# Optimization experiments

Hardware: AMD Instinct MI355X
Metric: run time of the kernel (lower is better)

Reference implementation:

```python
import jax, jax.numpy as jnp
import numpy as np
from functools import partial

NUM_PARTS = 6      # k clusters (PCB-style parts)
N_ITERS = 25       # fixed Lloyd iteration count (original uses tol=1e-4; fixed iters for jit/diff)


def _kmeans_single(points, k, n_iters):
    """Lloyd's k-means on points [N, D]; returns centers [k, D].
    Deterministic init: first k points (stand-in for the original's random init)."""
    centers0 = points[:k]  # [k, D]
    pt_sq = jnp.sum(points * points, axis=-1, keepdims=True)  # [N, 1]

    def step(centers, _):
        # squared euclidean distances [N, k] via GEMM
        c_sq = jnp.sum(centers * centers, axis=-1)            # [k]
        d = pt_sq - 2.0 * (points @ centers.T) + c_sq[None, :]
        assign = jnp.argmin(d, axis=-1)                       # [N]
        onehot = jax.nn.one_hot(assign, k, dtype=points.dtype)  # [N, k]
        counts = jnp.sum(onehot, axis=0)                      # [k]
        sums = onehot.T @ points                              # [k, D]
        new_centers = sums / jnp.maximum(counts, 1.0)[:, None]
        # keep old center for empty clusters
        new_centers = jnp.where(counts[:, None] > 0, new_centers, centers)
        return new_centers, None

    centers, _ = jax.lax.scan(step, centers0, None, length=n_iters)
    return centers  # [k, D]


def setup_inputs() -> dict:
    key = jax.random.key(0)
    x = jax.random.normal(key, (64, 2048, 24, 12), dtype=jnp.float32)
    return {"x": x}


def reference(x):
    B, C = x.shape[0], x.shape[1]
    pts = x.reshape(B, C, -1).transpose(0, 2, 1)              # [B, N=H*W, C]
    centers = jax.vmap(partial(_kmeans_single, k=NUM_PARTS, n_iters=N_ITERS))(pts)  # [B, k, C]
    clus = centers.transpose(0, 2, 1)[:, :, :, None]          # [B, C, k, 1]
    return clus
```

## Files before the change

### kernel.cpp

```cpp
#include <hip/hip_runtime.h>

#define NPTS 288
#define DIMS 2048
#define KC   6
#define N_IT 25

#define GT   96
#define KB   32
#define KSPL 2
#define KPS  (DIMS / KSPL)
#define NCH  (KPS / KB)
#define NTP  6

#define GLD16(gp, lp) __builtin_amdgcn_global_load_lds(                      \
    (const __attribute__((address_space(1))) void*)(gp),                     \
    (__attribute__((address_space(3))) void*)(lp), 16, 0, 0)

__global__ __launch_bounds__(256, 2) void k_gram(const float* __restrict__ x,
                                                 float* __restrict__ Gp, int nb) {
  const int bid = blockIdx.x;
  const int b  = bid / (NTP * KSPL);
  const int r0 = bid - b * (NTP * KSPL);
  const int ks = r0 / NTP, pr = r0 - ks * NTP;
  const int ti = (pr < 3) ? 0 : ((pr < 5) ? 1 : 2);
  const int tj = (pr < 3) ? pr : ((pr < 5) ? (pr - 2) : 2);
  const int t = threadIdx.x;
  const int tr = t >> 4, tc = t & 15;
  const int w = t >> 6, l = t & 63;
  const float* __restrict__ xb = x + (size_t)b * (DIMS * NPTS);
  float* __restrict__ Gb = Gp + ((size_t)ks * nb + b) * (NPTS * NPTS);

  __shared__ __attribute__((aligned(16))) float bufA[2][KB][GT];
  __shared__ __attribute__((aligned(16))) float bufB[2][KB][GT];

  int off[3];
#pragma unroll
  for (int iq = 0; iq < 3; ++iq) {
    const int e = (w * 3 + iq) * 256 + 4 * l;
    off[iq] = (e / GT) * NPTS + (e - (e / GT) * GT);
  }
  const float* __restrict__ baseA = xb + (size_t)(ks * KPS) * NPTS + ti * GT;
  const float* __restrict__ baseB = xb + (size_t)(ks * KPS) * NPTS + tj * GT;

  float acc[6][6];
#pragma unroll
  for (int ii = 0; ii < 6; ++ii)
#pragma unroll
    for (int jj = 0; jj < 6; ++jj) acc[ii][jj] = 0.f;

  auto stage = [&](int n, int c) {
#pragma unroll
    for (int iq = 0; iq < 3; ++iq) {
      const int o   = off[iq] + c * (KB * NPTS);
      const int lw  = (w * 3 + iq) * 256;
      GLD16(baseA + o, &bufA[n][0][0] + lw);
      GLD16(baseB + o, &bufB[n][0][0] + lw);
    }
  };

  stage(0, 0);
  __syncthreads();
  int n = 0;
  for (int c = 0; c < NCH; ++c) {
    if (c + 1 < NCH) stage(n ^ 1, c + 1);
#pragma unroll
    for (int kk = 0; kk < KB; ++kk) {
      float af[6], bf[6];
      const float2 a01 = *(const float2*)&bufA[n][kk][6 * tr];
      const float2 a23 = *(const float2*)&bufA[n][kk][6 * tr + 2];
      const float2 a45 = *(const float2*)&bufA[n][kk][6 * tr + 4];
      const float2 b01 = *(const float2*)&bufB[n][kk][6 * tc];
      const float2 b23 = *(const float2*)&bufB[n][kk][6 * tc + 2];
      const float2 b45 = *(const float2*)&bufB[n][kk][6 * tc + 4];
      af[0] = a01.x; af[1] = a01.y; af[2] = a23.x; af[3] = a23.y; af[4] = a45.x; af[5] = a45.y;
      bf[0] = b01.x; bf[1] = b01.y; bf[2] = b23.x; bf[3] = b23.y; bf[4] = b45.x; bf[5] = b45.y;
#pragma unroll
      for (int ii = 0; ii < 6; ++ii)
#pragma unroll
        for (int jj = 0; jj < 6; ++jj) acc[ii][jj] += af[ii] * bf[jj];
    }
    __syncthreads();
    n ^= 1;
  }

#pragma unroll
  for (int ii = 0; ii < 6; ++ii) {
    const int ri = ti * GT + 6 * tr + ii;
#pragma unroll
    for (int jj = 0; jj < 6; ++jj)
      Gb[(size_t)ri * NPTS + tj * GT + 6 * tc + jj] = acc[ii][jj];
  }
}

__global__ __launch_bounds__(256) void k_gsum(const float* __restrict__ Gp,
                                              float* __restrict__ G, int nb) {
  const size_t N2  = (size_t)NPTS * NPTS;
  const size_t tot = (size_t)nb * N2;
  const size_t p1  = (size_t)nb * N2;
  for (size_t e = (size_t)blockIdx.x * 256 + threadIdx.x; e < tot;
       e += (size_t)gridDim.x * 256) {
    const size_t b = e / N2;
    const int rc = (int)(e - b * N2);
    const int r = rc / NPTS, c = rc - r * NPTS;
    const int src_rc = ((r / GT) <= (c / GT)) ? rc : (c * NPTS + r);
    const size_t src = b * N2 + (size_t)src_rc;
    G[e] = Gp[src] + Gp[p1 + src];
  }
}

__global__ __launch_bounds__(1024) void k_lloyd(const float* __restrict__ G,
                                                float* __restrict__ wg, int nb) {
  const int b = blockIdx.x;
  const int t = threadIdx.x, wv = t >> 6, lane = t & 63;
  const float* __restrict__ Gb = G + (size_t)b * (NPTS * NPTS);

  __shared__ float w2[NPTS][8];
  __shared__ float pool[KC][NPTS][5];
  __shared__ float u[KC][NPTS];
  __shared__ int assign_s[NPTS];
  __shared__ float csq[KC];
  __shared__ int cnt_i[KC];

  for (int e = t; e < NPTS * 8; e += 1024) {
    const int i = e >> 3, k = e & 7;
    w2[i][k] = (k < KC && i == k) ? 1.f : 0.f;
  }
  __syncthreads();

  for (int it = 0; it < N_IT; ++it) {
    {
      const int jg = t / 320;
      const int i  = t - jg * 320;
      if (t < 960 && i < NPTS) {
        float a0 = 0, a1 = 0, a2 = 0, a3 = 0, a4 = 0, a5 = 0;
        const float* __restrict__ gp = Gb + (size_t)(jg * 96) * NPTS + i;
        for (int jj = 0; jj < 96; ++jj) {
          const float g = gp[(size_t)jj * NPTS];
          const int j = jg * 96 + jj;
          const float4 wA = *(const float4*)&w2[j][0];
          const float2 wB = *(const float2*)&w2[j][4];
          a0 += wA.x * g; a1 += wA.y * g; a2 += wA.z * g;
          a3 += wA.w * g; a4 += wB.x * g; a5 += wB.y * g;
        }
        pool[0][i][jg] = a0; pool[1][i][jg] = a1; pool[2][i][jg] = a2;
        pool[3][i][jg] = a3; pool[4][i][jg] = a4; pool[5][i][jg] = a5;
      }
    }
    __syncthreads();
    for (int e = t; e < KC * NPTS; e += 1024) {
      const int k = e / NPTS, i = e - k * NPTS;
      u[k][i] = pool[k][i][0] + pool[k][i][1] + pool[k][i][2];
    }
    if (t >= 960 && t < 960 + KC) cnt_i[t - 960] = 0;
    __syncthreads();
    if (wv < KC) {
      float s = 0.f;
      for (int i = lane; i < NPTS; i += 64) s += w2[i][wv] * u[wv][i];
#pragma unroll
      for (int off = 32; off; off >>= 1) s += __shfl_xor(s, off, 64);
      if (lane == 0) csq[wv] = s;
    }
    __syncthreads();
    int myA = -1;
    if (t < NPTS) {
      float best = 0.f;
      int bi = 0;
#pragma unroll
      for (int k = 0; k < KC; ++k) {
        const float sc = 0.5f * csq[k] - u[k][t];
        if (k == 0 || sc < best) { best = sc; bi = k; }
      }
      assign_s[t] = bi;
      myA = bi;
    }
    if (t < 320) {
#pragma unroll
      for (int k = 0; k < KC; ++k) {
        unsigned long long m = __ballot(myA == k);
        if (lane == 0) atomicAdd(&cnt_i[k], (int)__popcll(m));
      }
    }
    __syncthreads();
    if (t < NPTS) {
      const int a = assign_s[t];
#pragma unroll
      for (int k = 0; k < KC; ++k) {
        const int cn = cnt_i[k];
        if (cn > 0) w2[t][k] = (a == k) ? (1.0f / (float)cn) : 0.f;
      }
    }
    __syncthreads();
  }

  for (int e = t; e < NPTS * 8; e += 1024)
    wg[(size_t)b * (NPTS * 8) + e] = w2[e >> 3][e & 7];
}

__global__ __launch_bounds__(1024) void k_cent(const float* __restrict__ x,
                                               const float* __restrict__ wg,
                                               float* __restrict__ out, int nb) {
  const int b = blockIdx.x >> 3, s = blockIdx.x & 7;
  const int t = threadIdx.x, wv = t >> 6, lane = t & 63;
  const float* __restrict__ Mb = x + (size_t)b * (DIMS * NPTS);

  __shared__ float tile[64 * 145];
  __shared__ float pool[KC][64][17];
  __shared__ float w2[NPTS][8];

  for (int e = t; e < NPTS * 8; e += 1024)
    w2[e >> 3][e & 7] = wg[(size_t)b * (NPTS * 8) + e];

  for (int dt = 0; dt < 4; ++dt) {
    float a0 = 0, a1 = 0, a2 = 0, a3 = 0, a4 = 0, a5 = 0;
#pragma unroll
    for (int h = 0; h < 2; ++h) {
      __syncthreads();
#pragma unroll
      for (int i = 0; i < 9; ++i) {
        const int e = t + 1024 * i;
        const int d = e / 144, j = e - d * 144;
        tile[d * 145 + j] = Mb[(size_t)(s * 256 + dt * 64 + d) * NPTS + h * 144 + j];
      }
      __syncthreads();
      const int base = lane * 145 + wv * 9;
#pragma unroll
      for (int r = 0; r < 9; ++r) {
        const float p = tile[base + r];
        const int j = h * 144 + wv * 9 + r;
        const float4 wA = *(const float4*)&w2[j][0];
        const float2 wB = *(const float2*)&w2[j][4];
        a0 += wA.x * p; a1 += wA.y * p; a2 += wA.z * p;
        a3 += wA.w * p; a4 += wB.x * p; a5 += wB.y * p;
      }
    }
    pool[0][lane][wv] = a0; pool[1][lane][wv] = a1; pool[2][lane][wv] = a2;
    pool[3][lane][wv] = a3; pool[4][lane][wv] = a4; pool[5][lane][wv] = a5;
    __syncthreads();
    if (t < KC * 64) {
      const int d = t / KC, k = t - d * KC;
      float sum = 0.f;
#pragma unroll
      for (int w = 0; w < 16; ++w) sum += pool[k][d][w];
      out[((size_t)b * DIMS + s * 256 + dt * 64 + d) * KC + k] = sum;
    }
    __syncthreads();
  }
}

extern "C" void kernel_launch(void* const* d_in, const int* in_sizes, int n_in,
                              void* d_out, int out_size, void* d_ws, size_t ws_size,
                              hipStream_t stream) {
  const float* x = (const float*)d_in[0];
  float* out     = (float*)d_out;
  const int nb   = in_sizes[0] / (DIMS * NPTS);
  const size_t N2 = (size_t)NPTS * NPTS;

  float* Gp = (float*)d_ws;
  float* G  = Gp + (size_t)KSPL * nb * N2;
  float* wg = G + (size_t)nb * N2;

  hipLaunchKernelGGL(k_gram,  dim3(nb * NTP * KSPL), dim3(256),  0, stream, x, Gp, nb);
  hipLaunchKernelGGL(k_gsum,  dim3(4096),            dim3(256),  0, stream, Gp, G, nb);
  hipLaunchKernelGGL(k_lloyd, dim3(nb),              dim3(1024), 0, stream, G, wg, nb);
  hipLaunchKernelGGL(k_cent,  dim3(nb * 8),          dim3(1024), 0, stream, x, wg, out, nb);
}
```

Baseline: 475.8 us.

## Tile-based Gram symmetrization and assignment-indexed accumulation in Lloyd loop

k_gsum now works per 96x96 upper tile: it sums the split-K partials, writes the tile and writes its transpose through an LDS buffer, in place of a grid-stride loop with divides. The Lloyd matvec replaces the weight-matrix multiply with per-cluster accumulation keyed on a wave-uniform assignment (readfirstlane), and normalizes by precomputed reciprocal counts. The first iteration reads Gram columns directly. This relies on the assignment loaded being uniform across the wave, and on the hidden code staying consistent with the new count and normalization handling.

```diff
diff --git a/kernel.cpp b/kernel.cpp
--- a/kernel.cpp
+++ b/kernel.cpp
@@ -94,17 +94,35 @@
 
 __global__ __launch_bounds__(256) void k_gsum(const float* __restrict__ Gp,
                                               float* __restrict__ G, int nb) {
-  const size_t N2  = (size_t)NPTS * NPTS;
-  const size_t tot = (size_t)nb * N2;
-  const size_t p1  = (size_t)nb * N2;
-  for (size_t e = (size_t)blockIdx.x * 256 + threadIdx.x; e < tot;
-       e += (size_t)gridDim.x * 256) {
-    const size_t b = e / N2;
-    const int rc = (int)(e - b * N2);
-    const int r = rc / NPTS, c = rc - r * NPTS;
-    const int src_rc = ((r / GT) <= (c / GT)) ? rc : (c * NPTS + r);
-    const size_t src = b * N2 + (size_t)src_rc;
-    G[e] = Gp[src] + Gp[p1 + src];
+  const int bid = blockIdx.x;
+  const int b = bid / NTP, pr = bid - b * NTP;
+  const int ti = (pr < 3) ? 0 : ((pr < 5) ? 1 : 2);
+  const int tj = (pr < 3) ? pr : ((pr < 5) ? (pr - 2) : 2);
+  const int t = threadIdx.x;
+  const size_t N2 = (size_t)NPTS * NPTS;
+  const size_t p1 = (size_t)nb * N2;
+  const float* __restrict__ s0 = Gp + (size_t)b * N2;
+  const float* __restrict__ s1 = Gp + p1 + (size_t)b * N2;
+  float* __restrict__ Gb = G + (size_t)b * N2;
+
+  __shared__ float tl[GT * 97];
+
+#pragma unroll
+  for (int q = 0; q < 36; ++q) {
+    const int e = q * 256 + t;
+    const int lr = e / GT, lc = e - lr * GT;
+    const size_t idx = (size_t)(ti * GT + lr) * NPTS + tj * GT + lc;
+    const float v = s0[idx] + s1[idx];
+    Gb[idx] = v;
+    tl[lr * 97 + lc] = v;
+  }
+  if (ti == tj) return;
+  __syncthreads();
+#pragma unroll
+  for (int q = 0; q < 36; ++q) {
+    const int e = q * 256 + t;
+    const int lr = e / GT, lc = e - lr * GT;
+    Gb[(size_t)(tj * GT + lr) * NPTS + ti * GT + lc] = tl[lc * 97 + lr];
   }
 }
 
@@ -116,10 +134,12 @@
 
   __shared__ float w2[NPTS][8];
   __shared__ float pool[KC][NPTS][5];
-  __shared__ float u[KC][NPTS];
+  __shared__ float u[NPTS * KC > 0 ? KC : KC][NPTS];
   __shared__ int assign_s[NPTS];
   __shared__ float csq[KC];
   __shared__ int cnt_i[KC];
+  __shared__ float rn_s[KC];
+  __shared__ int live_s[KC];
 
   for (int e = t; e < NPTS * 8; e += 1024) {
     const int i = e >> 3, k = e & 7;
@@ -128,31 +148,50 @@
   __syncthreads();
 
   for (int it = 0; it < N_IT; ++it) {
-    {
+    if (t < KC) {
+      const int cn = cnt_i[t];
+      live_s[t] = (cn > 0) ? 1 : 0;
+      rn_s[t]   = (cn > 0) ? (1.0f / (float)cn) : 0.f;
+      cnt_i[t] = 0;
+    }
+    __syncthreads();
+
+    if (it == 0) {
+      if (t < NPTS) {
+#pragma unroll
+        for (int k = 0; k < KC; ++k) u[k][t] = Gb[(size_t)t * NPTS + k];
+      }
+    } else {
       const int jg = t / 320;
       const int i  = t - jg * 320;
       if (t < 960 && i < NPTS) {
-        float a0 = 0, a1 = 0, a2 = 0, a3 = 0, a4 = 0, a5 = 0;
+        float s0 = 0, s1 = 0, s2 = 0, s3 = 0, s4 = 0, s5 = 0;
         const float* __restrict__ gp = Gb + (size_t)(jg * 96) * NPTS + i;
+        const int jb = jg * 96;
         for (int jj = 0; jj < 96; ++jj) {
           const float g = gp[(size_t)jj * NPTS];
-          const int j = jg * 96 + jj;
-          const float4 wA = *(const float4*)&w2[j][0];
-          const float2 wB = *(const float2*)&w2[j][4];
-          a0 += wA.x * g; a1 += wA.y * g; a2 += wA.z * g;
-          a3 += wA.w * g; a4 += wB.x * g; a5 += wB.y * g;
+          const int a = __builtin_amdgcn_readfirstlane(assign_s[jb + jj]);
+          if      (a == 0) s0 += g;
+          else if (a == 1) s1 += g;
+          else if (a == 2) s2 += g;
+          else if (a == 3) s3 += g;
+          else if (a == 4) s4 += g;
+          else             s5 += g;
         }
-        pool[0][i][jg] = a0; pool[1][i][jg] = a1; pool[2][i][jg] = a2;
-        pool[3][i][jg] = a3; pool[4][i][jg] = a4; pool[5][i][jg] = a5;
-      }
-    }
-    __syncthreads();
-    for (int e = t; e < KC * NPTS; e += 1024) {
-      const int k = e / NPTS, i = e - k * NPTS;
-      u[k][i] = pool[k][i][0] + pool[k][i][1] + pool[k][i][2];
-    }
-    if (t >= 960 && t < 960 + KC) cnt_i[t - 960] = 0;
-    __syncthreads();
+        pool[0][i][jg] = s0; pool[1][i][jg] = s1; pool[2][i][jg] = s2;
+        pool[3][i][jg] = s3; pool[4][i][jg] = s4; pool[5][i][jg] = s5;
+      }
+    }
+    __syncthreads();
+    if (it > 0) {
+      for (int e = t; e < KC * NPTS; e += 1024) {
+        const int k = e / NPTS, i = e - k * NPTS;
+        if (live_s[k])
+          u[k][i] = (pool[k][i][0] + pool[k][i][1] + pool[k][i][2]) * rn_s[k];
+      }
+      __syncthreads();
+    }
+
     if (wv < KC) {
       float s = 0.f;
       for (int i = lane; i < NPTS; i += 64) s += w2[i][wv] * u[wv][i];
@@ -260,7 +299,7 @@
   float* wg = G + (size_t)nb * N2;
 
   hipLaunchKernelGGL(k_gram,  dim3(nb * NTP * KSPL), dim3(256),  0, stream, x, Gp, nb);
-  hipLaunchKernelGGL(k_gsum,  dim3(4096),            dim3(256),  0, stream, Gp, G, nb);
+  hipLaunchKernelGGL(k_gsum,  dim3(nb * NTP),        dim3(256),  0, stream, Gp, G, nb);
   hipLaunchKernelGGL(k_lloyd, dim3(nb),              dim3(1024), 0, stream, G, wg, nb);
   hipLaunchKernelGGL(k_cent,  dim3(nb * 8),          dim3(1024), 0, stream, x, wg, out, nb);
 }
```

Result: slower. 803.8 us (+68.9%).
